# Kernel tuning notes

Hardware: AMD Instinct MI355X
Metric: run time of the kernel (lower is better)

## Reference

```python
import jax, jax.numpy as jnp
import numpy as np
from jax import lax

N = 100000      # nodes
E = 1600000     # edges
T = 8           # timesteps
DS, DT = 10, 20 # static / temporal features
GH = 64         # gnn_hidden
LH = 64         # lstm_hidden
EC = 64         # end_channels
OC = 1          # out_channels
EPS = 1e-5


def setup_inputs() -> dict:
    key = jax.random.key(0)
    ks = jax.random.split(key, 20)
    g = lambda i, shape, s=0.05: jax.random.normal(ks[i], shape, jnp.float32) * s
    return {
        "x": jax.random.normal(ks[0], (N, DS + DT, T), jnp.float32),
        "edge_index": jax.random.randint(ks[1], (2, E), 0, N, jnp.int64),
        # static encoder (computed in forward but unused downstream, kept for faithfulness)
        "W_static": g(2, (GH, DS)), "b_static": g(3, (GH,)),
        # LSTMCell: input_size = DT + GH, hidden = LH; gate order i,f,g,o
        "W_ih": g(4, (4 * LH, DT + GH)), "W_hh": g(5, (4 * LH, LH)),
        "b_ih": g(6, (4 * LH,)), "b_hh": g(7, (4 * LH,)),
        # GraphConv(lstm_hidden -> gnn_hidden): lin_rel (with bias) on aggregated msgs + lin_root (no bias)
        "W_rel": g(8, (GH, LH)), "b_rel": g(9, (GH,)), "W_root": g(10, (GH, LH)),
        # BatchNorm1d(GH+LH)
        "gamma": jnp.ones((GH + LH,), jnp.float32), "beta": jnp.zeros((GH + LH,), jnp.float32),
        # head: linear1(128->EC), linear2(EC->128), output_layer(128->OC)
        "W1": g(11, (EC, GH + LH)), "b1": g(12, (EC,)),
        "W2": g(13, (GH + LH, EC)), "b2": g(14, (GH + LH,)),
        "W_out": g(15, (OC, GH + LH)), "b_out": g(16, (OC,)),
    }


def reference(x, edge_index, W_static, b_static, W_ih, W_hh, b_ih, b_hh,
              W_rel, b_rel, W_root, gamma, beta, W1, b1, W2, b2, W_out, b_out):
    src, dst = edge_index[0], edge_index[1]
    x_static = x[:, :DS, 0]                      # [N, DS]
    x_temporal = x[:, DS:DS + DT, :]             # [N, DT, T]
    static_embed = x_static @ W_static.T + b_static  # computed but unused (matches source)

    xt_seq = jnp.transpose(x_temporal, (2, 0, 1))  # [T, N, DT]
    h0 = jnp.zeros((N, GH), jnp.float32)
    c0 = jnp.zeros((N, GH), jnp.float32)

    def step(carry, x_t):
        h, c = carry
        # GraphConv: sum-aggregate neighbor h, then linear (linear commutes with sum)
        agg = jax.ops.segment_sum(h[src], dst, num_segments=N)   # [N, LH]
        gnn_out = agg @ W_rel.T + b_rel + h @ W_root.T           # [N, GH]
        inp = jnp.concatenate([x_t, gnn_out], axis=1)            # [N, DT+GH]
        gates = inp @ W_ih.T + b_ih + h @ W_hh.T + b_hh          # [N, 4*LH]
        i, f, g_, o = jnp.split(gates, 4, axis=1)
        c_new = jax.nn.sigmoid(f) * c + jax.nn.sigmoid(i) * jnp.tanh(g_)
        h_new = jax.nn.sigmoid(o) * jnp.tanh(c_new)
        return (h_new, c_new), gnn_out

    (h, c), gnn_outs = lax.scan(step, (h0, c0), xt_seq)
    gnn_out = gnn_outs[-1]  # gnn output computed at the last timestep (pre-update h)

    fused = jnp.concatenate([h, gnn_out], axis=1)                # [N, GH+LH]
    # BatchNorm1d, training-mode batch statistics (dropout p set to 0)
    mean = fused.mean(axis=0)
    var = fused.var(axis=0)
    normed = (fused - mean) * lax.rsqrt(var + EPS) * gamma + beta
    h1 = jax.nn.relu(normed @ W1.T + b1)
    hidden = jax.nn.relu(h1 @ W2.T + b2)
    out = jax.nn.sigmoid(hidden @ W_out.T + b_out)               # binary task -> sigmoid
    return out
```

## Files before the change

kernel.cpp:

```cpp
#include <hip/hip_runtime.h>

#define NN 100000
#define NE 1600000
#define TT 8
#define KF 160
#define XSTR 24
#define HISTB 6250
#define NRANGE 8
#define RSPAN 12500

typedef __attribute__((ext_vector_type(8))) short bf16x8;
typedef __attribute__((ext_vector_type(4))) float f32x4;
typedef unsigned int uint_;
typedef unsigned short ushort_;

__device__ __forceinline__ float sigf(float x) { return 1.f / (1.f + __expf(-x)); }
__device__ __forceinline__ float tanhf_(float x) { return 1.f - 2.f / (__expf(2.f * x) + 1.f); }
__device__ __forceinline__ ushort_ f2b(float f) {
    uint_ u = __float_as_uint(f);
    u += 0x7fff + ((u >> 16) & 1);
    return (ushort_)(u >> 16);
}
__device__ __forceinline__ float bl(uint_ u) { return __uint_as_float(u << 16); }
__device__ __forceinline__ float bh(uint_ u) { return __uint_as_float(u & 0xffff0000u); }
__device__ __forceinline__ void acc8(float* a, uint4 v) {
    a[0] += bl(v.x); a[1] += bh(v.x); a[2] += bl(v.y); a[3] += bh(v.y);
    a[4] += bl(v.z); a[5] += bh(v.z); a[6] += bl(v.w); a[7] += bh(v.w);
}
__device__ __forceinline__ uint_ pk(float a, float b) {
    return (uint_)f2b(a) | ((uint_)f2b(b) << 16);
}

__global__ void k_detect(const int* __restrict__ ei, int* flag) {
    int i = blockIdx.x * 256 + threadIdx.x;
    if (ei[2 * i + 1] != 0) atomicOr(flag, 1);
}

__global__ void k_hist_xt(const int* __restrict__ ei, const int* __restrict__ flag, int* cnt,
                          const float* __restrict__ x, ushort_* __restrict__ xT) {
    int b = blockIdx.x;
    if (b < HISTB) {
        int e = b * 256 + threadIdx.x;
        if (e >= NE) return;
        int is32 = *flag;
        int d = is32 ? ei[NE + e] : ei[2 * (NE + e)];
        atomicAdd(&cnt[d], 1);
    } else {
        if (!xT) return;
        int i = (b - HISTB) * 256 + threadIdx.x;
        if (i >= NN * XSTR) return;
        int n = i / XSTR, kk = i - n * XSTR;
        if (kk < 20) {
            const float* xp = x + (size_t)n * 240 + (10 + kk) * 8;
#pragma unroll
            for (int t = 0; t < 8; t++) xT[(size_t)t * NN * XSTR + i] = f2b(xp[t]);
        } else {
#pragma unroll
            for (int t = 0; t < 8; t++) xT[(size_t)t * NN * XSTR + i] = 0;
        }
    }
}

__global__ void k_scanblk(const int* __restrict__ cnt, int* off, int* bsum) {
    __shared__ int tmp[1024];
    int i = blockIdx.x * 1024 + threadIdx.x;
    int v = (i < NN) ? cnt[i] : 0;
    tmp[threadIdx.x] = v;
    __syncthreads();
    for (int d = 1; d < 1024; d <<= 1) {
        int t = (threadIdx.x >= d) ? tmp[threadIdx.x - d] : 0;
        __syncthreads();
        tmp[threadIdx.x] += t;
        __syncthreads();
    }
    if (i < NN) off[i + 1] = tmp[threadIdx.x];
    if (threadIdx.x == 1023) bsum[blockIdx.x] = tmp[1023];
}

__global__ void k_scantop(int* bsum, int nb) {
    if (threadIdx.x == 0) {
        int run = 0;
        for (int b = 0; b < nb; b++) { int t = bsum[b]; bsum[b] = run; run += t; }
    }
}

__global__ void k_scanadd(int* off, const int* __restrict__ bsum) {
    int i = blockIdx.x * 1024 + threadIdx.x;
    if (i < NN) off[i + 1] += bsum[blockIdx.x];
    if (i == 0) off[0] = 0;
}

__global__ void k_scatter(const int* __restrict__ ei, const int* __restrict__ flag,
                          int* cursor, int* csr) {
    int b = blockIdx.x;
    int range = b & (NRANGE - 1), chunk = b >> 3;
    int e = chunk * 256 + threadIdx.x;
    if (e >= NE) return;
    int is32 = *flag;
    int d = is32 ? ei[NE + e] : ei[2 * (NE + e)];
    if (d / RSPAN != range) return;
    int s = is32 ? ei[e] : ei[2 * e];
    int pos = atomicAdd(&cursor[d], 1);
    csr[pos] = s;
}

__global__ void k_prep(const float* __restrict__ W_ih, const float* __restrict__ W_hh,
                       const float* __restrict__ b_ih, const float* __restrict__ b_hh,
                       const float* __restrict__ W_rel, const float* __restrict__ b_rel,
                       const float* __restrict__ W_root, ushort_* WgB, float* bgp) {
    int n = threadIdx.x;
    int k = blockIdx.x;
    if (k < KF) {
        float v = 0.f;
        if (n < 256) {
            int w = n >> 6, g = (n >> 4) & 3, j = w * 16 + (n & 15);
            int row = g * 64 + j;
            if (k < 20) {
                v = W_ih[row * 84 + k];
            } else if (k >= 24 && k < 88) {
                int kk = k - 24;
                float a = 0.f;
                for (int m = 0; m < 64; m++) a += W_ih[row * 84 + 20 + m] * W_rel[m * 64 + kk];
                v = a;
            } else if (k >= 88 && k < 152) {
                int kk = k - 88;
                float a = W_hh[row * 64 + kk];
                for (int m = 0; m < 64; m++) a += W_ih[row * 84 + 20 + m] * W_root[m * 64 + kk];
                v = a;
            }
        } else {
            int j = n - 256;
            if (k >= 24 && k < 88) v = W_rel[j * 64 + (k - 24)];
            else if (k >= 88 && k < 152) v = W_root[j * 64 + (k - 88)];
        }
        WgB[(size_t)n * KF + k] = f2b(v);
    } else {
        if (n < 256) {
            int j = n >> 2, g = n & 3;
            int row = g * 64 + j;
            float a = b_ih[row] + b_hh[row];
            for (int m = 0; m < 64; m++) a += W_ih[row * 84 + 20 + m] * b_rel[m];
            bgp[n] = a;
        } else {
            bgp[n] = b_rel[n - 256];
        }
    }
}

template <bool LAST>
__device__ __forceinline__ void step_body(const float* __restrict__ x,
                                          const ushort_* __restrict__ xT,
                                          const int* __restrict__ off,
                                          const int* __restrict__ csr,
                                          const ushort_* __restrict__ hbR,
                                          ushort_* __restrict__ hbW,
                                          float* __restrict__ hf,
                                          float* __restrict__ c,
                                          const ushort_* __restrict__ WgB,
                                          const float* __restrict__ bgp,
                                          float* __restrict__ gnn,
                                          float* __restrict__ sums,
                                          float* __restrict__ sumsq, int t) {
    constexpr int NT = LAST ? 5 : 4;
    __shared__ __align__(16) ushort_ Zs[64 * 168];
    const int tid = threadIdx.x;
    const int nblk = blockIdx.x * 64;
    const int w = tid >> 6, lane = tid & 63;
    const int q = lane >> 4, l16 = lane & 15;

#pragma unroll
    for (int i = 0; i < 3; ++i) {
        int slot = tid + 256 * i;
        int n = slot / 12, oo = slot - n * 12;
        int n_g = nblk + n;
        uint4 z = make_uint4(0, 0, 0, 0);
        if (n_g < NN) {
            if (oo < 3) {
                if (xT) {
                    z = *(const uint4*)(xT + ((size_t)t * NN + n_g) * XSTR + oo * 8);
                } else {
                    const float* xp = x + (size_t)n_g * 240 + 80 + (size_t)oo * 64 + t;
                    uint_ r[4];
#pragma unroll
                    for (int p = 0; p < 4; p++) {
                        int k0 = oo * 8 + p * 2;
                        ushort_ b0 = (k0 < 20) ? f2b(xp[p * 16]) : (ushort_)0;
                        ushort_ b1 = (k0 + 1 < 20) ? f2b(xp[p * 16 + 8]) : (ushort_)0;
                        r[p] = (uint_)b0 | ((uint_)b1 << 16);
                    }
                    z = make_uint4(r[0], r[1], r[2], r[3]);
                }
            } else if (oo < 11) {
                z = *(const uint4*)(hbR + (size_t)n_g * 64 + (oo - 3) * 8);
            }
        }
        int oct = (oo < 3) ? oo : ((oo < 11) ? (oo + 8) : 19);
        *(uint4*)(Zs + n * 168 + oct * 8) = z;
    }

    {
        int slot = tid >> 3;
        int l8 = tid & 7;
        for (int nn = slot; nn < 64; nn += 32) {
            int node = nblk + nn;
            float a[8];
#pragma unroll
            for (int i = 0; i < 8; i++) a[i] = 0.f;
            if (t > 0 && node < NN) {
                int e0 = off[node], e1 = off[node + 1];
                int e = e0;
                for (; e + 8 <= e1; e += 8) {
                    uint4 v0 = *(const uint4*)(hbR + (size_t)csr[e] * 64 + l8 * 8);
                    uint4 v1 = *(const uint4*)(hbR + (size_t)csr[e + 1] * 64 + l8 * 8);
                    uint4 v2 = *(const uint4*)(hbR + (size_t)csr[e + 2] * 64 + l8 * 8);
                    uint4 v3 = *(const uint4*)(hbR + (size_t)csr[e + 3] * 64 + l8 * 8);
                    uint4 v4 = *(const uint4*)(hbR + (size_t)csr[e + 4] * 64 + l8 * 8);
                    uint4 v5 = *(const uint4*)(hbR + (size_t)csr[e + 5] * 64 + l8 * 8);
                    uint4 v6 = *(const uint4*)(hbR + (size_t)csr[e + 6] * 64 + l8 * 8);
                    uint4 v7 = *(const uint4*)(hbR + (size_t)csr[e + 7] * 64 + l8 * 8);
                    acc8(a, v0); acc8(a, v1); acc8(a, v2); acc8(a, v3);
                    acc8(a, v4); acc8(a, v5); acc8(a, v6); acc8(a, v7);
                }
                for (; e < e1; e++) {
                    uint4 v0 = *(const uint4*)(hbR + (size_t)csr[e] * 64 + l8 * 8);
                    acc8(a, v0);
                }
            }
            uint4 o;
            o.x = pk(a[0], a[1]); o.y = pk(a[2], a[3]);
            o.z = pk(a[4], a[5]); o.w = pk(a[6], a[7]);
            *(uint4*)(Zs + nn * 168 + 24 + l8 * 8) = o;
        }
    }
    __syncthreads();

    f32x4 acc[4][NT];
#pragma unroll
    for (int mt = 0; mt < 4; mt++)
#pragma unroll
        for (int nt = 0; nt < NT; nt++) acc[mt][nt] = (f32x4)(0.f);

#pragma unroll
    for (int kt = 0; kt < 5; ++kt) {
        bf16x8 af[4], bf[NT];
#pragma unroll
        for (int mt = 0; mt < 4; mt++)
            af[mt] = *(const bf16x8*)(Zs + (mt * 16 + l16) * 168 + kt * 32 + q * 8);
#pragma unroll
        for (int nt = 0; nt < NT; nt++) {
            int n = (nt < 4) ? (w * 64 + nt * 16 + l16) : (256 + w * 16 + l16);
            bf[nt] = *(const bf16x8*)(WgB + (size_t)n * KF + kt * 32 + q * 8);
        }
#pragma unroll
        for (int mt = 0; mt < 4; mt++)
#pragma unroll
            for (int nt = 0; nt < NT; nt++)
                acc[mt][nt] = __builtin_amdgcn_mfma_f32_16x16x32_bf16(af[mt], bf[nt], acc[mt][nt], 0, 0, 0);
    }

    const int j = w * 16 + l16;
    const f32x4 bias = *(const f32x4*)(bgp + j * 4);
    const float brl = LAST ? bgp[256 + j] : 0.f;
    float sh = 0.f, sh2 = 0.f, sg = 0.f, sg2 = 0.f;

    __syncthreads();
    ushort_* Hs   = Zs;
    float*   CsLo = (float*)(Zs + 4096);

    float cnHi[8];
#pragma unroll
    for (int mt = 0; mt < 4; ++mt) {
#pragma unroll
        for (int r = 0; r < 4; ++r) {
            int nloc = mt * 16 + q * 4 + r;
            int node = nblk + nloc;
            float cn = 0.f, hn = 0.f;
            if (node < NN) {
                size_t idx = (size_t)node * 64 + j;
                float iv = sigf(acc[mt][0][r] + bias.x);
                float fv = sigf(acc[mt][1][r] + bias.y);
                float gv = tanhf_(acc[mt][2][r] + bias.z);
                float ov = sigf(acc[mt][3][r] + bias.w);
                cn = fv * c[idx] + iv * gv;
                hn = ov * tanhf_(cn);
                if (LAST) {
                    float gn = acc[mt][4][r] + brl;
                    hf[idx] = hn;
                    gnn[idx] = gn;
                    sh += hn; sh2 += hn * hn;
                    sg += gn; sg2 += gn * gn;
                }
            }
            Hs[nloc * 64 + j] = f2b(hn);
            if (mt < 2) CsLo[nloc * 64 + j] = cn;
            else        cnHi[(mt - 2) * 4 + r] = cn;
        }
    }
    __syncthreads();
#pragma unroll
    for (int i = 0; i < 2; ++i) {
        int s = tid + 256 * i;
        {
            int n = s >> 3, part = s & 7;
            if (nblk + n < NN)
                *(uint4*)(hbW + (size_t)(nblk + n) * 64 + part * 8) =
                    *(const uint4*)(Hs + n * 64 + part * 8);
        }
        {
            int n = s >> 4, part = s & 15;
            if (nblk + n < NN)
                *(float4*)(c + (size_t)(nblk + n) * 64 + part * 4) =
                    *(const float4*)(CsLo + n * 64 + part * 4);
        }
    }
    __syncthreads();
    float* CsHi = (float*)Zs;
#pragma unroll
    for (int mt = 2; mt < 4; ++mt)
#pragma unroll
        for (int r = 0; r < 4; ++r) {
            int nloc = mt * 16 + q * 4 + r;
            CsHi[(nloc - 32) * 64 + j] = cnHi[(mt - 2) * 4 + r];
        }
    __syncthreads();
#pragma unroll
    for (int i = 0; i < 2; ++i) {
        int s = tid + 256 * i;
        int n = 32 + (s >> 4), part = s & 15;
        if (nblk + n < NN)
            *(float4*)(c + (size_t)(nblk + n) * 64 + part * 4) =
                *(const float4*)(CsHi + (n - 32) * 64 + part * 4);
    }

    if (LAST) {
#pragma unroll
        for (int d = 16; d < 64; d <<= 1) {
            sh += __shfl_xor(sh, d, 64);
            sh2 += __shfl_xor(sh2, d, 64);
            sg += __shfl_xor(sg, d, 64);
            sg2 += __shfl_xor(sg2, d, 64);
        }
        if (q == 0) {
            atomicAdd(&sums[j], sh);
            atomicAdd(&sumsq[j], sh2);
            atomicAdd(&sums[64 + j], sg);
            atomicAdd(&sumsq[64 + j], sg2);
        }
    }
}

__global__ __launch_bounds__(256, 4) void k_step(const float* __restrict__ x,
                                                 const ushort_* __restrict__ xT,
                                                 const int* __restrict__ off,
                                                 const int* __restrict__ csr,
                                                 const ushort_* __restrict__ hbR,
                                                 ushort_* __restrict__ hbW,
                                                 float* __restrict__ hf,
                                                 float* __restrict__ c,
                                                 const ushort_* __restrict__ WgB,
                                                 const float* __restrict__ bgp, int t) {
    step_body<false>(x, xT, off, csr, hbR, hbW, hf, c, WgB, bgp, nullptr, nullptr, nullptr, t);
}

__global__ __launch_bounds__(256, 4) void k_stepL(const float* __restrict__ x,
                                                  const ushort_* __restrict__ xT,
                                                  const int* __restrict__ off,
                                                  const int* __restrict__ csr,
                                                  const ushort_* __restrict__ hbR,
                                                  ushort_* __restrict__ hbW,
                                                  float* __restrict__ hf,
                                                  float* __restrict__ c,
                                                  const ushort_* __restrict__ WgB,
                                                  const float* __restrict__ bgp,
                                                  float* __restrict__ gnn,
                                                  float* __restrict__ sums,
                                                  float* __restrict__ sumsq, int t) {
    step_body<true>(x, xT, off, csr, hbR, hbW, hf, c, WgB, bgp, gnn, sums, sumsq, t);
}

__global__ __launch_bounds__(256) void k_head(const float* __restrict__ hf,
                                              const float* __restrict__ gnn,
                                              const float* __restrict__ sums,
                                              const float* __restrict__ sumsq,
                                              const float* __restrict__ gamma,
                                              const float* __restrict__ beta,
                                              const float* __restrict__ W1,
                                              const float* __restrict__ b1,
                                              const float* __restrict__ W2,
                                              const float* __restrict__ b2,
                                              const float* __restrict__ W_out,
                                              const float* __restrict__ b_out,
                                              float* __restrict__ out) {
    __shared__ __align__(16) ushort_ Zs[64 * 168];
    __shared__ __align__(16) ushort_ W1s[64 * 168];
    __shared__ __align__(16) ushort_ W2s[128 * 72];
    __shared__ __align__(16) ushort_ H1s[64 * 72];
    __shared__ float ab[256];
    __shared__ float Obuf[4][64];
    const int tid = threadIdx.x;
    const int w = tid >> 6, lane = tid & 63;
    const int q = lane >> 4, l16 = lane & 15;

    if (tid < 128) {
        float mean = sums[tid] / (float)NN;
        float var = sumsq[tid] / (float)NN - mean * mean;
        float a = gamma[tid] * rsqrtf(var + 1e-5f);
        ab[tid] = a;
        ab[128 + tid] = beta[tid] - mean * a;
    }
#pragma unroll
    for (int i = 0; i < 8; ++i) {
        int slot = tid + 256 * i;
        int jj = slot >> 5, k4 = slot & 31;
        float4 v = *(const float4*)(W1 + (size_t)jj * 128 + k4 * 4);
        *(uint2*)(W1s + jj * 168 + k4 * 4) = make_uint2(pk(v.x, v.y), pk(v.z, v.w));
    }
#pragma unroll
    for (int i = 0; i < 8; ++i) {
        int slot = tid + 256 * i;
        int jj = slot >> 4, k4 = slot & 15;
        float4 v = *(const float4*)(W2 + (size_t)jj * 64 + k4 * 4);
        *(uint2*)(W2s + jj * 72 + k4 * 4) = make_uint2(pk(v.x, v.y), pk(v.z, v.w));
    }
    const int j1 = w * 16 + l16;
    const float bb1 = b1[j1];
    const int j2a = (w * 2) * 16 + l16, j2b = (w * 2 + 1) * 16 + l16;
    const float bb2a = b2[j2a], bb2b = b2[j2b];
    const float woa = W_out[j2a], wob = W_out[j2b];
    const float bo = b_out[0];
    __syncthreads();

    const int NTILE = (NN + 63) / 64;
    for (int tile = blockIdx.x; tile < NTILE; tile += gridDim.x) {
        const int nblk = tile * 64;
#pragma unroll
        for (int i = 0; i < 8; ++i) {
            int slot = tid + 256 * i;
            int n = slot >> 5, f4 = slot & 31;
            int n_g = nblk + n;
            uint2 z = make_uint2(0, 0);
            if (n_g < NN) {
                const float* src = (f4 < 16) ? (hf + (size_t)n_g * 64 + f4 * 4)
                                             : (gnn + (size_t)n_g * 64 + (f4 - 16) * 4);
                float4 v = *(const float4*)src;
                int F = f4 * 4;
                z = make_uint2(pk(v.x * ab[F] + ab[128 + F], v.y * ab[F + 1] + ab[129 + F]),
                               pk(v.z * ab[F + 2] + ab[130 + F], v.w * ab[F + 3] + ab[131 + F]));
            }
            *(uint2*)(Zs + n * 168 + f4 * 4) = z;
        }
        __syncthreads();
        f32x4 acc1[4];
#pragma unroll
        for (int mt = 0; mt < 4; mt++) acc1[mt] = (f32x4)(0.f);
#pragma unroll
        for (int kt = 0; kt < 4; ++kt) {
            bf16x8 bfw = *(const bf16x8*)(W1s + j1 * 168 + kt * 32 + q * 8);
#pragma unroll
            for (int mt = 0; mt < 4; mt++) {
                bf16x8 af = *(const bf16x8*)(Zs + (mt * 16 + l16) * 168 + kt * 32 + q * 8);
                acc1[mt] = __builtin_amdgcn_mfma_f32_16x16x32_bf16(af, bfw, acc1[mt], 0, 0, 0);
            }
        }
#pragma unroll
        for (int mt = 0; mt < 4; mt++)
#pragma unroll
            for (int r = 0; r < 4; r++) {
                int nloc = mt * 16 + q * 4 + r;
                H1s[nloc * 72 + j1] = f2b(fmaxf(acc1[mt][r] + bb1, 0.f));
            }
        __syncthreads();
        f32x4 acc2[4][2];
#pragma unroll
        for (int mt = 0; mt < 4; mt++)
#pragma unroll
            for (int nt = 0; nt < 2; nt++) acc2[mt][nt] = (f32x4)(0.f);
#pragma unroll
        for (int kt = 0; kt < 2; ++kt) {
            bf16x8 bfa = *(const bf16x8*)(W2s + j2a * 72 + kt * 32 + q * 8);
            bf16x8 bfb = *(const bf16x8*)(W2s + j2b * 72 + kt * 32 + q * 8);
#pragma unroll
            for (int mt = 0; mt < 4; mt++) {
                bf16x8 af = *(const bf16x8*)(H1s + (mt * 16 + l16) * 72 + kt * 32 + q * 8);
                acc2[mt][0] = __builtin_amdgcn_mfma_f32_16x16x32_bf16(af, bfa, acc2[mt][0], 0, 0, 0);
                acc2[mt][1] = __builtin_amdgcn_mfma_f32_16x16x32_bf16(af, bfb, acc2[mt][1], 0, 0, 0);
            }
        }
#pragma unroll
        for (int mt = 0; mt < 4; mt++) {
#pragma unroll
            for (int r = 0; r < 4; r++) {
                float p = fmaxf(acc2[mt][0][r] + bb2a, 0.f) * woa +
                          fmaxf(acc2[mt][1][r] + bb2b, 0.f) * wob;
#pragma unroll
                for (int d = 1; d < 16; d <<= 1) p += __shfl_xor(p, d, 64);
                if (l16 == 0) Obuf[w][mt * 16 + q * 4 + r] = p;
            }
        }
        __syncthreads();
        if (tid < 64) {
            int n_g = nblk + tid;
            if (n_g < NN) {
                float s = Obuf[0][tid] + Obuf[1][tid] + Obuf[2][tid] + Obuf[3][tid];
                out[n_g] = sigf(s + bo);
            }
        }
        __syncthreads();
    }
}

extern "C" void kernel_launch(void* const* d_in, const int* in_sizes, int n_in,
                              void* d_out, int out_size, void* d_ws, size_t ws_size,
                              hipStream_t stream) {
    const float* x      = (const float*)d_in[0];
    const int*   ei     = (const int*)d_in[1];
    const float* W_ih   = (const float*)d_in[4];
    const float* W_hh   = (const float*)d_in[5];
    const float* b_ih   = (const float*)d_in[6];
    const float* b_hh   = (const float*)d_in[7];
    const float* W_rel  = (const float*)d_in[8];
    const float* b_rel  = (const float*)d_in[9];
    const float* W_root = (const float*)d_in[10];
    const float* gamma  = (const float*)d_in[11];
    const float* beta   = (const float*)d_in[12];
    const float* W1     = (const float*)d_in[13];
    const float* b1     = (const float*)d_in[14];
    const float* W2     = (const float*)d_in[15];
    const float* b2     = (const float*)d_in[16];
    const float* W_out  = (const float*)d_in[17];
    const float* b_out  = (const float*)d_in[18];
    float* out = (float*)d_out;

    char* ws = (char*)d_ws;
    size_t o = 0;
    auto carve = [&](size_t bytes) { char* p = ws + o; o += (bytes + 255) & ~(size_t)255; return p; };
    int*     off   = (int*)carve((NN + 1) * 4);
    int*     cnt   = (int*)carve(NN * 4);
    int*     bsum  = (int*)carve(128 * 4);
    int*     flag  = (int*)carve(256);
    int*     csr   = (int*)carve((size_t)NE * 4);
    float*   hf    = (float*)carve((size_t)NN * 64 * 4);
    float*   c     = (float*)carve((size_t)NN * 64 * 4);
    float*   gnn   = (float*)carve((size_t)NN * 64 * 4);
    ushort_* hbA   = (ushort_*)carve((size_t)NN * 64 * 2);
    ushort_* hbB   = (ushort_*)carve((size_t)NN * 64 * 2);
    ushort_* WgB   = (ushort_*)carve((size_t)320 * KF * 2);
    float*   bgp   = (float*)carve(320 * 4);
    float*   sums  = (float*)carve(128 * 4);
    float*   sumsq = (float*)carve(128 * 4);
    ushort_* xT = nullptr;
    size_t need_xt = (size_t)TT * NN * XSTR * 2;
    if (o + need_xt + 256 <= ws_size) xT = (ushort_*)carve(need_xt);

    const int nscan = (NN + 1023) / 1024;
    const int xtb = xT ? (NN * XSTR + 255) / 256 : 0;

    hipMemsetAsync(flag, 0, 4, stream);
    hipMemsetAsync(cnt, 0, NN * 4, stream);
    k_detect<<<16, 256, 0, stream>>>(ei, flag);
    k_hist_xt<<<HISTB + xtb, 256, 0, stream>>>(ei, flag, cnt, x, xT);
    k_scanblk<<<nscan, 1024, 0, stream>>>(cnt, off, bsum);
    k_scantop<<<1, 64, 0, stream>>>(bsum, nscan);
    k_scanadd<<<nscan, 1024, 0, stream>>>(off, bsum);
    hipMemcpyAsync(cnt, off, NN * 4, hipMemcpyDeviceToDevice, stream);
    k_scatter<<<(NE / 256) * NRANGE, 256, 0, stream>>>(ei, flag, cnt, csr);

    hipMemsetAsync(c, 0, (size_t)NN * 64 * 4, stream);
    hipMemsetAsync(hbA, 0, (size_t)NN * 64 * 2, stream);
    hipMemsetAsync(sums, 0, 1024, stream);
    k_prep<<<KF + 1, 320, 0, stream>>>(W_ih, W_hh, b_ih, b_hh, W_rel, b_rel, W_root, WgB, bgp);

    const int ngates = (NN + 63) / 64;
    for (int t = 0; t < TT; ++t) {
        ushort_* hbR = (t & 1) ? hbB : hbA;
        ushort_* hbW = (t & 1) ? hbA : hbB;
        if (t == TT - 1)
            k_stepL<<<ngates, 256, 0, stream>>>(x, xT, off, csr, hbR, hbW, hf, c,
                                                WgB, bgp, gnn, sums, sumsq, t);
        else
            k_step<<<ngates, 256, 0, stream>>>(x, xT, off, csr, hbR, hbW, hf, c,
                                               WgB, bgp, t);
    }

    k_head<<<512, 256, 0, stream>>>(hf, gnn, sums, sumsq, gamma, beta,
                                    W1, b1, W2, b2, W_out, b_out, out);
}
```

Measured before the change: 918.7 us.

## Balance edge aggregation per block with packed dst tags and LDS atomics

The CSR entries now pack the source index with the low 6 bits of the destination node. Each block's edge range is then split evenly across 32 thread groups, which removes the per-node imbalance of degree-varying loops. Partial sums are flushed into a float LDS buffer with shared atomics whenever the destination changes, then packed to bf16. The same LDS buffer is reused to stage the c state, which simplifies the split c writeback. In exchange the kernel uses about 16KB more shared memory, which may lower occupancy, and adds LDS atomic traffic.

New measurement: 1.005 ms. 9.4% more time.

```diff
diff --git a/kernel.cpp b/kernel.cpp
--- a/kernel.cpp
+++ b/kernel.cpp
@@ -8,6 +8,7 @@
 #define HISTB 6250
 #define NRANGE 8
 #define RSPAN 12500
+#define SMASK 0x03FFFFFFu
 
 typedef __attribute__((ext_vector_type(8))) short bf16x8;
 typedef __attribute__((ext_vector_type(4))) float f32x4;
@@ -91,7 +92,7 @@
 }
 
 __global__ void k_scatter(const int* __restrict__ ei, const int* __restrict__ flag,
-                          int* cursor, int* csr) {
+                          int* cursor, uint_* csr) {
     int b = blockIdx.x;
     int range = b & (NRANGE - 1), chunk = b >> 3;
     int e = chunk * 256 + threadIdx.x;
@@ -101,7 +102,7 @@
     if (d / RSPAN != range) return;
     int s = is32 ? ei[e] : ei[2 * e];
     int pos = atomicAdd(&cursor[d], 1);
-    csr[pos] = s;
+    csr[pos] = (uint_)s | ((uint_)(d & 63) << 26);
 }
 
 __global__ void k_prep(const float* __restrict__ W_ih, const float* __restrict__ W_hh,
@@ -151,7 +152,7 @@
 __device__ __forceinline__ void step_body(const float* __restrict__ x,
                                           const ushort_* __restrict__ xT,
                                           const int* __restrict__ off,
-                                          const int* __restrict__ csr,
+                                          const uint_* __restrict__ csr,
                                           const ushort_* __restrict__ hbR,
                                           ushort_* __restrict__ hbW,
                                           float* __restrict__ hf,
@@ -163,10 +164,15 @@
                                           float* __restrict__ sumsq, int t) {
     constexpr int NT = LAST ? 5 : 4;
     __shared__ __align__(16) ushort_ Zs[64 * 168];
+    __shared__ __align__(16) float aggF[64 * 64];
     const int tid = threadIdx.x;
     const int nblk = blockIdx.x * 64;
     const int w = tid >> 6, lane = tid & 63;
     const int q = lane >> 4, l16 = lane & 15;
+
+#pragma unroll
+    for (int i = 0; i < 4; ++i)
+        *(float4*)(aggF + (tid + 256 * i) * 4) = make_float4(0.f, 0.f, 0.f, 0.f);
 
 #pragma unroll
     for (int i = 0; i < 3; ++i) {
@@ -197,40 +203,69 @@
         int oct = (oo < 3) ? oo : ((oo < 11) ? (oo + 8) : 19);
         *(uint4*)(Zs + n * 168 + oct * 8) = z;
     }
+    __syncthreads();
+
+    if (t > 0) {
+        const int g = tid >> 3, l8 = tid & 7;
+        const int e0 = off[nblk];
+        const int eEnd = off[(nblk + 64 < NN) ? (nblk + 64) : NN];
+        const int nE = eEnd - e0;
+        const int cs = (nE + 31) >> 5;
+        int myS = e0 + g * cs;
+        int myE = myS + cs; if (myE > eEnd) myE = eEnd;
+        float a[8];
+#pragma unroll
+        for (int i = 0; i < 8; i++) a[i] = 0.f;
+        int cur = -1;
+        for (int base = myS; base < myE; base += 8) {
+            uint_ vv[8];
+            uint4 rr[8];
+#pragma unroll
+            for (int k = 0; k < 8; k++) {
+                int e = base + k;
+                vv[k] = (e < myE) ? csr[e] : 0u;
+            }
+#pragma unroll
+            for (int k = 0; k < 8; k++) {
+                int e = base + k;
+                rr[k] = (e < myE)
+                    ? *(const uint4*)(hbR + (size_t)(vv[k] & SMASK) * 64 + l8 * 8)
+                    : make_uint4(0, 0, 0, 0);
+            }
+#pragma unroll
+            for (int k = 0; k < 8; k++) {
+                int e = base + k;
+                if (e < myE) {
+                    int d = (int)(vv[k] >> 26);
+                    if (d != cur) {
+                        if (cur >= 0) {
+#pragma unroll
+                            for (int f = 0; f < 8; f++) {
+                                atomicAdd(&aggF[cur * 64 + l8 * 8 + f], a[f]);
+                                a[f] = 0.f;
+                            }
+                        }
+                        cur = d;
+                    }
+                    acc8(a, rr[k]);
+                }
+            }
+        }
+        if (cur >= 0) {
+#pragma unroll
+            for (int f = 0; f < 8; f++) atomicAdd(&aggF[cur * 64 + l8 * 8 + f], a[f]);
+        }
+    }
+    __syncthreads();
 
     {
-        int slot = tid >> 3;
-        int l8 = tid & 7;
-        for (int nn = slot; nn < 64; nn += 32) {
-            int node = nblk + nn;
-            float a[8];
-#pragma unroll
-            for (int i = 0; i < 8; i++) a[i] = 0.f;
-            if (t > 0 && node < NN) {
-                int e0 = off[node], e1 = off[node + 1];
-                int e = e0;
-                for (; e + 8 <= e1; e += 8) {
-                    uint4 v0 = *(const uint4*)(hbR + (size_t)csr[e] * 64 + l8 * 8);
-                    uint4 v1 = *(const uint4*)(hbR + (size_t)csr[e + 1] * 64 + l8 * 8);
-                    uint4 v2 = *(const uint4*)(hbR + (size_t)csr[e + 2] * 64 + l8 * 8);
-                    uint4 v3 = *(const uint4*)(hbR + (size_t)csr[e + 3] * 64 + l8 * 8);
-                    uint4 v4 = *(const uint4*)(hbR + (size_t)csr[e + 4] * 64 + l8 * 8);
-                    uint4 v5 = *(const uint4*)(hbR + (size_t)csr[e + 5] * 64 + l8 * 8);
-                    uint4 v6 = *(const uint4*)(hbR + (size_t)csr[e + 6] * 64 + l8 * 8);
-                    uint4 v7 = *(const uint4*)(hbR + (size_t)csr[e + 7] * 64 + l8 * 8);
-                    acc8(a, v0); acc8(a, v1); acc8(a, v2); acc8(a, v3);
-                    acc8(a, v4); acc8(a, v5); acc8(a, v6); acc8(a, v7);
-                }
-                for (; e < e1; e++) {
-                    uint4 v0 = *(const uint4*)(hbR + (size_t)csr[e] * 64 + l8 * 8);
-                    acc8(a, v0);
-                }
-            }
-            uint4 o;
-            o.x = pk(a[0], a[1]); o.y = pk(a[2], a[3]);
-            o.z = pk(a[4], a[5]); o.w = pk(a[6], a[7]);
-            *(uint4*)(Zs + nn * 168 + 24 + l8 * 8) = o;
-        }
+        int n = tid >> 2, fq = (tid & 3) * 16;
+        const float* src = aggF + n * 64 + fq;
+        uint_ p[8];
+#pragma unroll
+        for (int i = 0; i < 8; i++) p[i] = pk(src[2 * i], src[2 * i + 1]);
+        *(uint4*)(Zs + n * 168 + 24 + fq) = make_uint4(p[0], p[1], p[2], p[3]);
+        *(uint4*)(Zs + n * 168 + 24 + fq + 8) = make_uint4(p[4], p[5], p[6], p[7]);
     }
     __syncthreads();
 
@@ -265,9 +300,8 @@
 
     __syncthreads();
     ushort_* Hs   = Zs;
-    float*   CsLo = (float*)(Zs + 4096);
-
-    float cnHi[8];
+    float*   Cs   = aggF;
+
 #pragma unroll
     for (int mt = 0; mt < 4; ++mt) {
 #pragma unroll
@@ -292,44 +326,25 @@
                 }
             }
             Hs[nloc * 64 + j] = f2b(hn);
-            if (mt < 2) CsLo[nloc * 64 + j] = cn;
-            else        cnHi[(mt - 2) * 4 + r] = cn;
+            Cs[nloc * 64 + j] = cn;
         }
     }
     __syncthreads();
 #pragma unroll
     for (int i = 0; i < 2; ++i) {
         int s = tid + 256 * i;
-        {
-            int n = s >> 3, part = s & 7;
-            if (nblk + n < NN)
-                *(uint4*)(hbW + (size_t)(nblk + n) * 64 + part * 8) =
-                    *(const uint4*)(Hs + n * 64 + part * 8);
-        }
-        {
-            int n = s >> 4, part = s & 15;
-            if (nblk + n < NN)
-                *(float4*)(c + (size_t)(nblk + n) * 64 + part * 4) =
-                    *(const float4*)(CsLo + n * 64 + part * 4);
-        }
-    }
-    __syncthreads();
-    float* CsHi = (float*)Zs;
-#pragma unroll
-    for (int mt = 2; mt < 4; ++mt)
-#pragma unroll
-        for (int r = 0; r < 4; ++r) {
-            int nloc = mt * 16 + q * 4 + r;
-            CsHi[(nloc - 32) * 64 + j] = cnHi[(mt - 2) * 4 + r];
-        }
-    __syncthreads();
-#pragma unroll
-    for (int i = 0; i < 2; ++i) {
+        int n = s >> 3, part = s & 7;
+        if (nblk + n < NN)
+            *(uint4*)(hbW + (size_t)(nblk + n) * 64 + part * 8) =
+                *(const uint4*)(Hs + n * 64 + part * 8);
+    }
+#pragma unroll
+    for (int i = 0; i < 4; ++i) {
         int s = tid + 256 * i;
-        int n = 32 + (s >> 4), part = s & 15;
+        int n = s >> 4, part = s & 15;
         if (nblk + n < NN)
             *(float4*)(c + (size_t)(nblk + n) * 64 + part * 4) =
-                *(const float4*)(CsHi + (n - 32) * 64 + part * 4);
+                *(const float4*)(Cs + n * 64 + part * 4);
     }
 
     if (LAST) {
@@ -352,7 +367,7 @@
 __global__ __launch_bounds__(256, 4) void k_step(const float* __restrict__ x,
                                                  const ushort_* __restrict__ xT,
                                                  const int* __restrict__ off,
-                                                 const int* __restrict__ csr,
+                                                 const uint_* __restrict__ csr,
                                                  const ushort_* __restrict__ hbR,
                                                  ushort_* __restrict__ hbW,
                                                  float* __restrict__ hf,
@@ -365,7 +380,7 @@
 __global__ __launch_bounds__(256, 4) void k_stepL(const float* __restrict__ x,
                                                   const ushort_* __restrict__ xT,
                                                   const int* __restrict__ off,
-                                                  const int* __restrict__ csr,
+                                                  const uint_* __restrict__ csr,
                                                   const ushort_* __restrict__ hbR,
                                                   ushort_* __restrict__ hbW,
                                                   float* __restrict__ hf,
@@ -538,7 +553,7 @@
     int*     cnt   = (int*)carve(NN * 4);
     int*     bsum  = (int*)carve(128 * 4);
     int*     flag  = (int*)carve(256);
-    int*     csr   = (int*)carve((size_t)NE * 4);
+    uint_*   csr   = (uint_*)carve((size_t)NE * 4);
     float*   hf    = (float*)carve((size_t)NN * 64 * 4);
     float*   c     = (float*)carve((size_t)NN * 64 * 4);
     float*   gnn   = (float*)carve((size_t)NN * 64 * 4);
```
